# Kernel tuning notes

Measured on AMD Instinct MI355X. Metric: run time of the kernel, lower is better.

## Reference

```python
import jax, jax.numpy as jnp
import numpy as np

B, S, D = 8, 4096, 1024
E, R, K = 6, 16, 2


def setup_inputs() -> dict:
    key = jax.random.key(0)
    ks = jax.random.split(key, 9)
    sc = 0.02
    return {
        "x": jax.random.normal(ks[0], (B, S, D), jnp.float32),
        "base_W": jax.random.normal(ks[1], (D, D), jnp.float32) * sc,
        "base_b": jax.random.normal(ks[2], (D,), jnp.float32) * sc,
        "shared_A": jax.random.normal(ks[3], (R, D), jnp.float32) * sc,
        "shared_B": jax.random.normal(ks[4], (D, R), jnp.float32) * sc,
        "routed_A": jax.random.normal(ks[5], (E, R, D), jnp.float32) * sc,
        "routed_B": jax.random.normal(ks[6], (E, D, R), jnp.float32) * sc,
        "router_W": jax.random.normal(ks[7], (E, D), jnp.float32) * sc,
        "router_b": jax.random.normal(ks[8], (E,), jnp.float32) * sc,
    }


def reference(x, base_W, base_b, shared_A, shared_B, routed_A, routed_B, router_W, router_b):
    # Frozen base linear (torch.no_grad in the original)
    base_out = jax.lax.stop_gradient(jnp.einsum("bsi,oi->bso", x, base_W) + base_b)

    # Shared expert (num_shared = 1): low-rank in->rank->out
    shared_out = jnp.einsum("bsr,or->bso", jnp.einsum("bsi,ri->bsr", x, shared_A), shared_B)

    # Router: softmax over experts, top-k, scatter back to sparse weights, renormalize
    logits = jnp.einsum("bsi,ei->bse", x, router_W) + router_b
    gate = jax.nn.softmax(logits, axis=-1)                      # [B,S,E]
    topk_w, topk_i = jax.lax.top_k(gate, K)                     # [B,S,K]
    sparse_w = jnp.sum(jax.nn.one_hot(topk_i, E, dtype=gate.dtype) * topk_w[..., None], axis=-2)  # [B,S,E]
    sparse_w = sparse_w / (jnp.sum(sparse_w, axis=-1, keepdims=True) + 1e-6)

    # Dense compute of all routed experts (faithful to the torch.stack), then weighted combine
    h = jnp.einsum("bsi,eri->bser", x, routed_A)                # [B,S,E,R]
    routed_outs = jnp.einsum("bser,eor->bseo", h, routed_B)     # [B,S,E,out]
    routed_out = jnp.einsum("bseo,bse->bso", routed_outs, sparse_w)

    return base_out + shared_out + routed_out
```

## Files before the change

kernel.cpp:

```cpp
#include <hip/hip_runtime.h>
#include <hip/hip_bf16.h>

typedef unsigned short u16;
typedef __attribute__((ext_vector_type(8))) __bf16 bf16x8;
typedef __attribute__((ext_vector_type(8))) unsigned short u16x8;
typedef __attribute__((ext_vector_type(4))) float f32x4;

#define NTOK 32768
#define XLDA 1152
#define WS_XU  0
#define WS_WP  75497472
#define WS_W1T 77856768

static __device__ __forceinline__ u16 f2bf(float f) {
  __hip_bfloat16 h = __float2bfloat16(f);
  return __builtin_bit_cast(u16, h);
}

#define GLOAD_LDS16(g, l)                                                     \
  __builtin_amdgcn_global_load_lds(                                           \
      (const __attribute__((address_space(1))) void*)(g),                     \
      (__attribute__((address_space(3))) void*)(l), 16, 0, 0)

__global__ __launch_bounds__(256) void pack_weights(
    const float* __restrict__ baseW, const float* __restrict__ sharedA,
    const float* __restrict__ sharedB, const float* __restrict__ routedA,
    const float* __restrict__ routedB,
    u16* __restrict__ Wp, u16* __restrict__ W1t) {
  int idx = blockIdx.x * 256 + threadIdx.x;
  const int NWP = 1024 * 1152;
  if (idx < NWP) {
    int o = idx / 1152, k = idx - o * 1152;
    float v;
    if (k < 1024)      v = baseW[o * 1024 + k];
    else if (k < 1040) v = sharedB[o * 16 + (k - 1024)];
    else if (k < 1136) { int c = k - 1040; v = routedB[((c >> 4) * 1024 + o) * 16 + (c & 15)]; }
    else               v = 0.0f;
    Wp[idx] = f2bf(v);
  } else {
    int j = idx - NWP;
    int n = j >> 10, k = j & 1023;
    float v;
    if (n < 16)       v = sharedA[n * 1024 + k];
    else if (n < 112) v = routedA[(n - 16) * 1024 + k];
    else              v = 0.0f;
    W1t[j] = f2bf(v);
  }
}

__global__ __launch_bounds__(256) void expert_fused(
    const float* __restrict__ x, const float* __restrict__ rW, const float* __restrict__ rB,
    const u16* __restrict__ W1t, u16* __restrict__ xu) {
  __shared__ float rWs[6 * 1024];
  __shared__ u16 As[32 * 64];
  __shared__ u16 Bs[128 * 64];
  __shared__ float wspS[32][8];
  const int tid = threadIdx.x, lane = tid & 63, wid = tid >> 6;
  const int T0 = blockIdx.x * 32;
  const int r = tid >> 3, kc = tid & 7;
  const int srow = lane >> 3, scol8 = (lane & 7) * 8;
  const int fr = lane & 15, fq = lane >> 4;

  for (int i = tid; i < 1536; i += 256)
    ((float4*)rWs)[i] = ((const float4*)rW)[i];

  float lp[6];
  #pragma unroll
  for (int e = 0; e < 6; ++e) lp[e] = 0.f;
  f32x4 acc[2][2];
  #pragma unroll
  for (int m = 0; m < 2; ++m)
    #pragma unroll
    for (int n = 0; n < 2; ++n) acc[m][n] = f32x4{0.f, 0.f, 0.f, 0.f};

  for (int kt = 0; kt < 16; ++kt) {
    __syncthreads();
    #pragma unroll
    for (int i = 0; i < 4; ++i) {
      int rr = wid * 32 + i * 8;
      GLOAD_LDS16(W1t + (size_t)(rr + srow) * 1024 + kt * 64 + scol8,
                  (char*)Bs + rr * 128);
    }
    const float4* p = (const float4*)(x + (size_t)(T0 + r) * 1024 + kt * 64 + kc * 8);
    float4 v0 = p[0], v1 = p[1];
    u16x8 o;
    o[0] = f2bf(v0.x); o[1] = f2bf(v0.y); o[2] = f2bf(v0.z); o[3] = f2bf(v0.w);
    o[4] = f2bf(v1.x); o[5] = f2bf(v1.y); o[6] = f2bf(v1.z); o[7] = f2bf(v1.w);
    *(u16x8*)&As[r * 64 + kc * 8] = o;
    *(u16x8*)&xu[(size_t)(T0 + r) * XLDA + kt * 64 + kc * 8] = o;
    {
      int kb = kt * 64 + kc * 8;
      #pragma unroll
      for (int e = 0; e < 6; ++e) {
        float4 w0 = *(const float4*)&rWs[e * 1024 + kb];
        float4 w1 = *(const float4*)&rWs[e * 1024 + kb + 4];
        lp[e] += v0.x * w0.x + v0.y * w0.y + v0.z * w0.z + v0.w * w0.w
               + v1.x * w1.x + v1.y * w1.y + v1.z * w1.z + v1.w * w1.w;
      }
    }
    __syncthreads();
    #pragma unroll
    for (int ks = 0; ks < 2; ++ks) {
      bf16x8 af[2], bv[2];
      #pragma unroll
      for (int m = 0; m < 2; ++m)
        af[m] = *(const bf16x8*)&As[(m * 16 + fr) * 64 + ks * 32 + fq * 8];
      #pragma unroll
      for (int n = 0; n < 2; ++n)
        bv[n] = *(const bf16x8*)&Bs[(wid * 32 + n * 16 + fr) * 64 + ks * 32 + fq * 8];
      #pragma unroll
      for (int m = 0; m < 2; ++m)
        #pragma unroll
        for (int n = 0; n < 2; ++n)
          acc[m][n] = __builtin_amdgcn_mfma_f32_16x16x32_bf16(af[m], bv[n], acc[m][n], 0, 0, 0);
    }
  }

  #pragma unroll
  for (int m = 1; m <= 4; m <<= 1)
    #pragma unroll
    for (int e = 0; e < 6; ++e)
      lp[e] += __shfl_xor(lp[e], m);

  if ((tid & 7) == 0) {
    float lg[6];
    #pragma unroll
    for (int e = 0; e < 6; ++e) lg[e] = lp[e] + rB[e];
    float mx = lg[0];
    #pragma unroll
    for (int e = 1; e < 6; ++e) mx = fmaxf(mx, lg[e]);
    float ex[6], ssum = 0.f;
    #pragma unroll
    for (int e = 0; e < 6; ++e) { ex[e] = __expf(lg[e] - mx); ssum += ex[e]; }
    float inv = 1.0f / ssum;
    int i1 = 0; float v1 = ex[0];
    #pragma unroll
    for (int e = 1; e < 6; ++e) if (ex[e] > v1) { v1 = ex[e]; i1 = e; }
    int i2 = -1; float v2 = -1.0f;
    #pragma unroll
    for (int e = 0; e < 6; ++e) if (e != i1 && ex[e] > v2) { v2 = ex[e]; i2 = e; }
    float g1 = v1 * inv, g2 = v2 * inv;
    float den = g1 + g2 + 1e-6f;
    #pragma unroll
    for (int e = 0; e < 6; ++e)
      wspS[r][e] = (e == i1) ? g1 / den : ((e == i2) ? g2 / den : 0.0f);
  }
  __syncthreads();

  #pragma unroll
  for (int n = 0; n < 2; ++n) {
    int col = wid * 32 + n * 16 + fr;
    int e = (col - 16) >> 4;
    #pragma unroll
    for (int m = 0; m < 2; ++m) {
      #pragma unroll
      for (int g = 0; g < 4; ++g) {
        int row = m * 16 + fq * 4 + g;
        float f = (col < 16) ? 1.0f : ((col < 112) ? wspS[row][e] : 0.0f);
        xu[(size_t)(T0 + row) * XLDA + 1024 + col] = f2bf(acc[m][n][g] * f);
      }
    }
  }
}

#define VMW()  asm volatile("s_waitcnt vmcnt(4)" ::: "memory")
#define VMW0() asm volatile("s_waitcnt vmcnt(0)" ::: "memory")
#define LGW()  asm volatile("s_waitcnt lgkmcnt(0)" ::: "memory")
#define BAR()  __builtin_amdgcn_s_barrier()

__global__ __launch_bounds__(512, 2) void gemm256(
    const u16* __restrict__ A, const u16* __restrict__ B,
    float* __restrict__ out, const float* __restrict__ bias) {
  extern __shared__ char lds[];
  const int lda = XLDA, ldb = XLDA;
  const int tid = threadIdx.x, lane = tid & 63, wid = tid >> 6;
  const int wr = wid >> 2, wcn = wid & 3;

  int bid = blockIdx.x;
  int xcd = bid & 7, idx = bid >> 3;
  int bx = xcd * 16 + (idx >> 2);
  int by = idx & 3;
  const int rowbase = bx * 256, colbase = by * 256;

  f32x4 acc[8][4];
  #pragma unroll
  for (int m = 0; m < 8; ++m)
    #pragma unroll
    for (int n = 0; n < 4; ++n) acc[m][n] = f32x4{0.f, 0.f, 0.f, 0.f};

  const int l3 = lane >> 3, l7 = lane & 7;
  const int kperm = ((l7 ^ l3) << 3);
  const u16* aSrc = A + (size_t)(rowbase + wr * 128 + wcn * 16 + l3) * lda + kperm;
  const int aDst = (wr * 128 + wcn * 16) * 128;
  const int bh = wcn >> 1, bq = wcn & 1;
  const u16* bSrc = B + (size_t)(colbase + bh * 128 + wr * 64 + bq * 16 + l3) * ldb + kperm;
  const int bDst = (bh * 128 + wr * 64 + bq * 16) * 128;

#define STAGE_A(bufp, kt, g) do {                                   \
    const u16* _s = aSrc + (g) * 64 * lda + (kt) * 64;              \
    char* _d = lds + (bufp) * 65536 + aDst + (g) * 64 * 128;        \
    GLOAD_LDS16(_s, _d);                                            \
    GLOAD_LDS16(_s + 8 * lda, _d + 8 * 128);                        \
  } while (0)
#define STAGE_B(bufp, kt, g) do {                                   \
    const u16* _s = bSrc + (g) * 32 * ldb + (kt) * 64;              \
    char* _d = lds + (bufp) * 65536 + 32768 + bDst + (g) * 32 * 128;\
    GLOAD_LDS16(_s, _d);                                            \
    GLOAD_LDS16(_s + 8 * ldb, _d + 8 * 128);                        \
  } while (0)

  const int fr = lane & 15, fq = lane >> 4;
  const int sswz = (lane & 7) << 4;

  auto LDA_ = [&](int bufp, int mh, bf16x8* a) {
    const char* base = lds + bufp * 65536 + (wr * 128 + mh * 64 + fr) * 128;
    #pragma unroll
    for (int m = 0; m < 4; ++m)
      #pragma unroll
      for (int ks = 0; ks < 2; ++ks)
        a[m * 2 + ks] = *(const bf16x8*)(base + m * 16 * 128 + ((ks * 64 + fq * 16) ^ sswz));
  };
  auto LDB_ = [&](int bufp, int nh, bf16x8* b) {
    const char* base = lds + bufp * 65536 + 32768 + (wcn * 64 + nh * 32 + fr) * 128;
    #pragma unroll
    for (int n = 0; n < 2; ++n)
      #pragma unroll
      for (int ks = 0; ks < 2; ++ks)
        b[n * 2 + ks] = *(const bf16x8*)(base + n * 16 * 128 + ((ks * 64 + fq * 16) ^ sswz));
  };
  auto MF = [&](bf16x8* a, bf16x8* b, int mo, int no) {
    __builtin_amdgcn_s_setprio(1);
    #pragma unroll
    for (int m = 0; m < 4; ++m)
      #pragma unroll
      for (int n = 0; n < 2; ++n)
        #pragma unroll
        for (int ks = 0; ks < 2; ++ks)
          acc[mo + m][no + n] = __builtin_amdgcn_mfma_f32_16x16x32_bf16(
              a[m * 2 + ks], b[n * 2 + ks], acc[mo + m][no + n], 0, 0, 0);
    __builtin_amdgcn_s_setprio(0);
  };

  STAGE_A(0, 0, 0); STAGE_B(0, 0, 0); STAGE_B(0, 0, 1); STAGE_A(0, 0, 1);
  VMW0(); BAR();

  bf16x8 a[8], b0[4], b1[4];
  for (int t = 0; t < 9; ++t) {
    LDA_(0, 0, a); LDB_(0, 0, b0);
    STAGE_A(1, 2 * t + 1, 0);
    VMW(); BAR(); LGW();
    MF(a, b0, 0, 0); BAR();

    LDB_(0, 1, b1);
    STAGE_B(1, 2 * t + 1, 0);
    VMW(); BAR(); LGW();
    MF(a, b1, 0, 2); BAR();

    LDA_(0, 1, a);
    STAGE_B(1, 2 * t + 1, 1);
    VMW(); BAR(); LGW();
    MF(a, b1, 4, 2); BAR();

    STAGE_A(1, 2 * t + 1, 1);
    VMW(); BAR();
    MF(a, b0, 4, 0); BAR();

    LDA_(1, 0, a); LDB_(1, 0, b0);
    if (t < 8) STAGE_A(0, 2 * t + 2, 0);
    VMW(); BAR(); LGW();
    MF(a, b0, 0, 0); BAR();

    LDB_(1, 1, b1);
    if (t < 8) STAGE_B(0, 2 * t + 2, 0);
    VMW(); BAR(); LGW();
    MF(a, b1, 0, 2); BAR();

    LDA_(1, 1, a);
    if (t < 8) STAGE_B(0, 2 * t + 2, 1);
    VMW(); BAR(); LGW();
    MF(a, b1, 4, 2); BAR();

    if (t < 8) STAGE_A(0, 2 * t + 2, 1);
    VMW(); BAR();
    MF(a, b0, 4, 0); BAR();
  }

  int row0 = rowbase + wr * 128 + (fq << 2);
  int col0 = colbase + wcn * 64 + fr;
  #pragma unroll
  for (int n = 0; n < 4; ++n) {
    int col = col0 + n * 16;
    float bv = bias[col];
    #pragma unroll
    for (int m = 0; m < 8; ++m) {
      int rb = row0 + m * 16;
      #pragma unroll
      for (int r = 0; r < 4; ++r)
        out[(size_t)(rb + r) * 1024 + col] = acc[m][n][r] + bv;
    }
  }
#undef STAGE_A
#undef STAGE_B
}

extern "C" void kernel_launch(void* const* d_in, const int* in_sizes, int n_in,
                              void* d_out, int out_size, void* d_ws, size_t ws_size,
                              hipStream_t stream) {
  const float* x       = (const float*)d_in[0];
  const float* baseW   = (const float*)d_in[1];
  const float* baseb   = (const float*)d_in[2];
  const float* sharedA = (const float*)d_in[3];
  const float* sharedB = (const float*)d_in[4];
  const float* routedA = (const float*)d_in[5];
  const float* routedB = (const float*)d_in[6];
  const float* routerW = (const float*)d_in[7];
  const float* routerb = (const float*)d_in[8];
  float* out = (float*)d_out;
  char* ws = (char*)d_ws;
  u16* xu  = (u16*)(ws + WS_XU);
  u16* Wp  = (u16*)(ws + WS_WP);
  u16* W1t = (u16*)(ws + WS_W1T);

  hipFuncSetAttribute((const void*)gemm256,
                      hipFuncAttributeMaxDynamicSharedMemorySize, 131072);

  pack_weights<<<5120, 256, 0, stream>>>(baseW, sharedA, sharedB, routedA, routedB,
                                         Wp, W1t);
  expert_fused<<<1024, 256, 0, stream>>>(x, routerW, routerb, W1t, xu);
  gemm256<<<dim3(512, 1), 512, 131072, stream>>>(xu, Wp, out, baseb);
}
```

Measured before the change: 158.8 us.

## Rewrite expert pre-pass as per-wave 16-token tiles without LDS or barriers

The expert/router pre-pass kernel now gives each wavefront its own 16 tokens, loading x and W1t fragments straight from global memory into MFMA operands instead of staging them through shared memory behind block barriers. The next x tile is prefetched into registers, router logits are reduced with cross-lane shuffles, and gate weights are broadcast by shuffle rather than through LDS. This removes barriers and LDS traffic but makes every wave re-read the full W1t and router weights from global/L2, adding redundant cache traffic.

```diff
diff --git a/kernel.cpp b/kernel.cpp
--- a/kernel.cpp
+++ b/kernel.cpp
@@ -48,81 +48,81 @@
   }
 }
 
-__global__ __launch_bounds__(256) void expert_fused(
-    const float* __restrict__ x, const float* __restrict__ rW, const float* __restrict__ rB,
-    const u16* __restrict__ W1t, u16* __restrict__ xu) {
-  __shared__ float rWs[6 * 1024];
-  __shared__ u16 As[32 * 64];
-  __shared__ u16 Bs[128 * 64];
-  __shared__ float wspS[32][8];
+__global__ __launch_bounds__(256) void fuse_wave(
+    const float* __restrict__ x, const float* __restrict__ rW,
+    const float* __restrict__ rB, const u16* __restrict__ W1t,
+    u16* __restrict__ xu) {
   const int tid = threadIdx.x, lane = tid & 63, wid = tid >> 6;
-  const int T0 = blockIdx.x * 32;
-  const int r = tid >> 3, kc = tid & 7;
-  const int srow = lane >> 3, scol8 = (lane & 7) * 8;
   const int fr = lane & 15, fq = lane >> 4;
-
-  for (int i = tid; i < 1536; i += 256)
-    ((float4*)rWs)[i] = ((const float4*)rW)[i];
+  const int T0 = (blockIdx.x * 4 + wid) * 16;
 
   float lp[6];
   #pragma unroll
   for (int e = 0; e < 6; ++e) lp[e] = 0.f;
-  f32x4 acc[2][2];
-  #pragma unroll
-  for (int m = 0; m < 2; ++m)
-    #pragma unroll
-    for (int n = 0; n < 2; ++n) acc[m][n] = f32x4{0.f, 0.f, 0.f, 0.f};
+  f32x4 acc[8];
+  #pragma unroll
+  for (int n = 0; n < 8; ++n) acc[n] = f32x4{0.f, 0.f, 0.f, 0.f};
+
+  const float* xrow  = x  + (size_t)(T0 + fr) * 1024 + fq * 8;
+  u16*         xurow = xu + (size_t)(T0 + fr) * XLDA + fq * 8;
+  const u16*   wbase = W1t + (size_t)fr * 1024 + fq * 8;
+  const float* rwb   = rW + fq * 8;
+
+  float4 c00 = *(const float4*)(xrow + 0);
+  float4 c01 = *(const float4*)(xrow + 4);
+  float4 c10 = *(const float4*)(xrow + 32);
+  float4 c11 = *(const float4*)(xrow + 36);
 
   for (int kt = 0; kt < 16; ++kt) {
-    __syncthreads();
-    #pragma unroll
-    for (int i = 0; i < 4; ++i) {
-      int rr = wid * 32 + i * 8;
-      GLOAD_LDS16(W1t + (size_t)(rr + srow) * 1024 + kt * 64 + scol8,
-                  (char*)Bs + rr * 128);
+    const int kn = (kt < 15 ? (kt + 1) * 64 : 15 * 64);
+    float4 n00 = *(const float4*)(xrow + kn + 0);
+    float4 n01 = *(const float4*)(xrow + kn + 4);
+    float4 n10 = *(const float4*)(xrow + kn + 32);
+    float4 n11 = *(const float4*)(xrow + kn + 36);
+
+    u16x8 o0, o1;
+    o0[0] = f2bf(c00.x); o0[1] = f2bf(c00.y); o0[2] = f2bf(c00.z); o0[3] = f2bf(c00.w);
+    o0[4] = f2bf(c01.x); o0[5] = f2bf(c01.y); o0[6] = f2bf(c01.z); o0[7] = f2bf(c01.w);
+    o1[0] = f2bf(c10.x); o1[1] = f2bf(c10.y); o1[2] = f2bf(c10.z); o1[3] = f2bf(c10.w);
+    o1[4] = f2bf(c11.x); o1[5] = f2bf(c11.y); o1[6] = f2bf(c11.z); o1[7] = f2bf(c11.w);
+    *(u16x8*)(xurow + kt * 64)      = o0;
+    *(u16x8*)(xurow + kt * 64 + 32) = o1;
+
+    #pragma unroll
+    for (int e = 0; e < 6; ++e) {
+      const float* w = rwb + e * 1024 + kt * 64;
+      float4 w00 = *(const float4*)(w + 0);
+      float4 w01 = *(const float4*)(w + 4);
+      float4 w10 = *(const float4*)(w + 32);
+      float4 w11 = *(const float4*)(w + 36);
+      lp[e] += c00.x * w00.x + c00.y * w00.y + c00.z * w00.z + c00.w * w00.w
+             + c01.x * w01.x + c01.y * w01.y + c01.z * w01.z + c01.w * w01.w
+             + c10.x * w10.x + c10.y * w10.y + c10.z * w10.z + c10.w * w10.w
+             + c11.x * w11.x + c11.y * w11.y + c11.z * w11.z + c11.w * w11.w;
     }
-    const float4* p = (const float4*)(x + (size_t)(T0 + r) * 1024 + kt * 64 + kc * 8);
-    float4 v0 = p[0], v1 = p[1];
-    u16x8 o;
-    o[0] = f2bf(v0.x); o[1] = f2bf(v0.y); o[2] = f2bf(v0.z); o[3] = f2bf(v0.w);
-    o[4] = f2bf(v1.x); o[5] = f2bf(v1.y); o[6] = f2bf(v1.z); o[7] = f2bf(v1.w);
-    *(u16x8*)&As[r * 64 + kc * 8] = o;
-    *(u16x8*)&xu[(size_t)(T0 + r) * XLDA + kt * 64 + kc * 8] = o;
-    {
-      int kb = kt * 64 + kc * 8;
-      #pragma unroll
-      for (int e = 0; e < 6; ++e) {
-        float4 w0 = *(const float4*)&rWs[e * 1024 + kb];
-        float4 w1 = *(const float4*)&rWs[e * 1024 + kb + 4];
-        lp[e] += v0.x * w0.x + v0.y * w0.y + v0.z * w0.z + v0.w * w0.w
-               + v1.x * w1.x + v1.y * w1.y + v1.z * w1.z + v1.w * w1.w;
-      }
+
+    bf16x8 a0 = __builtin_bit_cast(bf16x8, o0);
+    bf16x8 a1 = __builtin_bit_cast(bf16x8, o1);
+    #pragma unroll
+    for (int n = 0; n < 8; ++n) {
+      const u16* wp = wbase + n * 16 * 1024 + kt * 64;
+      bf16x8 b0 = *(const bf16x8*)(wp);
+      bf16x8 b1 = *(const bf16x8*)(wp + 32);
+      acc[n] = __builtin_amdgcn_mfma_f32_16x16x32_bf16(a0, b0, acc[n], 0, 0, 0);
+      acc[n] = __builtin_amdgcn_mfma_f32_16x16x32_bf16(a1, b1, acc[n], 0, 0, 0);
     }
-    __syncthreads();
-    #pragma unroll
-    for (int ks = 0; ks < 2; ++ks) {
-      bf16x8 af[2], bv[2];
-      #pragma unroll
-      for (int m = 0; m < 2; ++m)
-        af[m] = *(const bf16x8*)&As[(m * 16 + fr) * 64 + ks * 32 + fq * 8];
-      #pragma unroll
-      for (int n = 0; n < 2; ++n)
-        bv[n] = *(const bf16x8*)&Bs[(wid * 32 + n * 16 + fr) * 64 + ks * 32 + fq * 8];
-      #pragma unroll
-      for (int m = 0; m < 2; ++m)
-        #pragma unroll
-        for (int n = 0; n < 2; ++n)
-          acc[m][n] = __builtin_amdgcn_mfma_f32_16x16x32_bf16(af[m], bv[n], acc[m][n], 0, 0, 0);
-    }
-  }
-
-  #pragma unroll
-  for (int m = 1; m <= 4; m <<= 1)
-    #pragma unroll
-    for (int e = 0; e < 6; ++e)
-      lp[e] += __shfl_xor(lp[e], m);
-
-  if ((tid & 7) == 0) {
+
+    c00 = n00; c01 = n01; c10 = n10; c11 = n11;
+  }
+
+  #pragma unroll
+  for (int e = 0; e < 6; ++e) {
+    lp[e] += __shfl_xor(lp[e], 16);
+    lp[e] += __shfl_xor(lp[e], 32);
+  }
+
+  float wsp[6];
+  {
     float lg[6];
     #pragma unroll
     for (int e = 0; e < 6; ++e) lg[e] = lp[e] + rB[e];
@@ -143,22 +143,23 @@
     float den = g1 + g2 + 1e-6f;
     #pragma unroll
     for (int e = 0; e < 6; ++e)
-      wspS[r][e] = (e == i1) ? g1 / den : ((e == i2) ? g2 / den : 0.0f);
-  }
-  __syncthreads();
-
-  #pragma unroll
-  for (int n = 0; n < 2; ++n) {
-    int col = wid * 32 + n * 16 + fr;
-    int e = (col - 16) >> 4;
-    #pragma unroll
-    for (int m = 0; m < 2; ++m) {
-      #pragma unroll
-      for (int g = 0; g < 4; ++g) {
-        int row = m * 16 + fq * 4 + g;
-        float f = (col < 16) ? 1.0f : ((col < 112) ? wspS[row][e] : 0.0f);
-        xu[(size_t)(T0 + row) * XLDA + 1024 + col] = f2bf(acc[m][n][g] * f);
-      }
+      wsp[e] = (e == i1) ? g1 / den : ((e == i2) ? g2 / den : 0.0f);
+  }
+
+  float wg[4][6];
+  #pragma unroll
+  for (int g = 0; g < 4; ++g)
+    #pragma unroll
+    for (int e = 0; e < 6; ++e)
+      wg[g][e] = __shfl(wsp[e], fq * 4 + g);
+
+  #pragma unroll
+  for (int n = 0; n < 8; ++n) {
+    int col = n * 16 + fr;
+    #pragma unroll
+    for (int g = 0; g < 4; ++g) {
+      float f = (n == 0) ? 1.0f : ((n < 7) ? wg[g][n - 1] : 0.0f);
+      xu[(size_t)(T0 + fq * 4 + g) * XLDA + 1024 + col] = f2bf(acc[n][g] * f);
     }
   }
 }
@@ -326,6 +327,6 @@
 
   pack_weights<<<5120, 256, 0, stream>>>(baseW, sharedA, sharedB, routedA, routedB,
                                          Wp, W1t);
-  expert_fused<<<1024, 256, 0, stream>>>(x, routerW, routerb, W1t, xu);
+  fuse_wave<<<512, 256, 0, stream>>>(x, routerW, routerb, W1t, xu);
   gemm256<<<dim3(512, 1), 512, 131072, stream>>>(xu, Wp, out, baseb);
 }
```

After: 207.8 us. 30.8% more time.
